# Kernel optimization log

Measured on AMD Instinct MI355X. Metric: run time of the kernel, lower is better.

Reference implementation:

```python
import jax, jax.numpy as jnp
import numpy as np
from jax import lax

B, N, M, K = 8, 4096, 2048, 64   # graphs, points/graph, fps centers/graph (ratio=0.5), max neighbors
R = 0.5                           # radius
F_IN = 64


def setup_inputs() -> dict:
    key = jax.random.key(0)
    ks = jax.random.split(key, 6)
    x = jax.random.normal(ks[0], (B * N, F_IN), jnp.float32)
    pos = jax.random.normal(ks[1], (B * N, 3), jnp.float32)
    batch = jnp.repeat(jnp.arange(B, dtype=jnp.int32), N)  # sorted graph ids
    def lin_w(k, fi, fo):
        return (jax.random.normal(k, (fi, fo), jnp.float32) / np.sqrt(fi)).astype(jnp.float32)
    w1 = lin_w(ks[2], F_IN + 3, 64); b1 = jnp.zeros((64,), jnp.float32)
    w2 = lin_w(ks[3], 64, 64);       b2 = jnp.zeros((64,), jnp.float32)
    w3 = lin_w(ks[4], 64, 128);      b3 = jnp.zeros((128,), jnp.float32)
    return dict(x=x, pos=pos, batch=batch, w1=w1, b1=b1, w2=w2, b2=b2, w3=w3, b3=b3)


def fps(pos_g, m):
    """Farthest point sampling on one graph [n,3] -> m int32 indices (deterministic start at 0)."""
    n = pos_g.shape[0]
    def step(carry, _):
        mind, last = carry
        d = jnp.sum((pos_g - pos_g[last]) ** 2, axis=-1)
        mind = jnp.minimum(mind, d)
        return (mind, jnp.argmax(mind).astype(jnp.int32)), last
    init = (jnp.full((n,), 1e30, jnp.float32), jnp.int32(0))
    _, idx = lax.scan(step, init, None, length=m)
    return idx


def reference(x, pos, batch, w1, b1, w2, b2, w3, b3):
    # batch is sorted with equal-size graphs -> reshape to [B, N, .]
    pos_b = pos.reshape(B, N, 3)
    x_b = x.reshape(B, N, F_IN)

    # fps per graph (PyG.fps with ratio=0.5)
    cidx = jax.vmap(lambda p: fps(p, M))(pos_b)                 # [B, M]
    bi = jnp.arange(B)[:, None]
    pos_c = pos_b[bi, cidx]                                     # [B, M, 3]

    # radius ball query, capped at K neighbors (take K nearest, mask > R)
    d2 = jnp.sum((pos_c[:, :, None, :] - pos_b[:, None, :, :]) ** 2, axis=-1)  # [B, M, N]
    neg_d2k, nbr = lax.top_k(-d2, K)                            # [B, M, K]
    mask = (-neg_d2k) <= R * R                                  # center itself always valid (d=0)

    # PointConv message: nn(concat[x_j, pos_j - pos_i]), then max-aggregate per center
    bii = jnp.arange(B)[:, None, None]
    x_j = x_b[bii, nbr]                                         # [B, M, K, F_IN]
    rel = pos_b[bii, nbr] - pos_c[:, :, None, :]                # [B, M, K, 3]
    h = jnp.concatenate([x_j, rel], axis=-1)                    # [B, M, K, F_IN+3]
    h = jax.nn.relu(h @ w1 + b1)
    h = jax.nn.relu(h @ w2 + b2)
    h = h @ w3 + b3                                             # [B, M, K, 128]
    h = jnp.where(mask[..., None], h, -jnp.inf)
    out = jnp.max(h, axis=2)                                    # [B, M, 128]

    out_x = out.reshape(B * M, 128)
    out_pos = pos_c.reshape(B * M, 3)
    out_batch = jnp.repeat(jnp.arange(B, dtype=jnp.int32), M)
    return out_x, out_pos, out_batch
```

## Files before the change

kernel.cpp:

```cpp
#include <hip/hip_runtime.h>

#define BG 8
#define NP 4096
#define MC 2048
#define KN 64
#define NWK 248
#define CAND 480

__device__ __forceinline__ float dist2(float ax, float ay, float az,
                                       float bx, float by, float bz) {
    float dx = __fsub_rn(ax, bx), dy = __fsub_rn(ay, by), dz = __fsub_rn(az, bz);
    return __fadd_rn(__fadd_rn(__fmul_rn(dx, dx), __fmul_rn(dy, dy)), __fmul_rn(dz, dz));
}

template <int CTRL>
__device__ __forceinline__ float dppmax(float v) {
    int t = __builtin_amdgcn_update_dpp(0, __float_as_int(v), CTRL, 0xf, 0xf, true);
    return fmaxf(v, __int_as_float(t));
}

__global__ __launch_bounds__(256) void k_pre(
    const float* __restrict__ x, const float* __restrict__ w1, const float* __restrict__ b1,
    float* __restrict__ y)
{
    __shared__ float smem[8384];
    const int tid = threadIdx.x;
    const int p0 = blockIdx.x * 64;
    float* xs = smem;
    float* wsm = smem + 4160;
    float* bsm = smem + 8256;
    for (int i = tid; i < 4096; i += 256) {
        xs[(i >> 6) * 65 + (i & 63)] = x[(size_t)p0 * 64 + i];
        wsm[i] = w1[i];
    }
    if (tid < 64) bsm[tid] = b1[tid];
    __syncthreads();
    const int pl = tid >> 2, oq = tid & 3;
    float acc[16];
    #pragma unroll
    for (int u = 0; u < 16; u++) acc[u] = bsm[oq * 16 + u];
    for (int f = 0; f < 64; f++) {
        float xv = xs[pl * 65 + f];
        const float4* wp = (const float4*)&wsm[f * 64 + oq * 16];
        float4 a = wp[0], b4 = wp[1], c4 = wp[2], d4 = wp[3];
        acc[0] = fmaf(xv, a.x, acc[0]);   acc[1] = fmaf(xv, a.y, acc[1]);
        acc[2] = fmaf(xv, a.z, acc[2]);   acc[3] = fmaf(xv, a.w, acc[3]);
        acc[4] = fmaf(xv, b4.x, acc[4]);  acc[5] = fmaf(xv, b4.y, acc[5]);
        acc[6] = fmaf(xv, b4.z, acc[6]);  acc[7] = fmaf(xv, b4.w, acc[7]);
        acc[8] = fmaf(xv, c4.x, acc[8]);  acc[9] = fmaf(xv, c4.y, acc[9]);
        acc[10] = fmaf(xv, c4.z, acc[10]); acc[11] = fmaf(xv, c4.w, acc[11]);
        acc[12] = fmaf(xv, d4.x, acc[12]); acc[13] = fmaf(xv, d4.y, acc[13]);
        acc[14] = fmaf(xv, d4.z, acc[14]); acc[15] = fmaf(xv, d4.w, acc[15]);
    }
    float4* yo = (float4*)&y[((size_t)p0 + pl) * 64 + oq * 16];
    yo[0] = make_float4(acc[0], acc[1], acc[2], acc[3]);
    yo[1] = make_float4(acc[4], acc[5], acc[6], acc[7]);
    yo[2] = make_float4(acc[8], acc[9], acc[10], acc[11]);
    yo[3] = make_float4(acc[12], acc[13], acc[14], acc[15]);
}

__global__ __launch_bounds__(512, 2) void k_fused(
    const float* __restrict__ pos, const float* __restrict__ y,
    const float* __restrict__ w1, const float* __restrict__ w2, const float* __restrict__ b2,
    const float* __restrict__ w3, const float* __restrict__ b3,
    float* __restrict__ out_pos, float* __restrict__ out_batch, float* __restrict__ out_x,
    int* __restrict__ prog)
{
    __shared__ float smem[12320];
    const int tid = threadIdx.x;
    if (blockIdx.x < BG) {
        const int b = blockIdx.x;
        const float* pg = pos + (size_t)b * NP * 3;
        for (int i = tid; i < NP * 3; i += 512) smem[i] = pg[i];
        __syncthreads();
        const int lane = tid & 63, wv = tid >> 6;
        float px[8], py[8], pz[8], mind[8];
        const int base = tid * 8;
        #pragma unroll
        for (int i = 0; i < 8; i++) {
            px[i] = smem[(base + i) * 3];
            py[i] = smem[(base + i) * 3 + 1];
            pz[i] = smem[(base + i) * 3 + 2];
            mind[i] = 1e30f;
        }
        float2* sl = (float2*)(smem + NP * 3);
        float cx = smem[0], cy = smem[1], cz = smem[2];
        if (tid == 0) {
            const size_t c3 = (size_t)b * MC * 3;
            __hip_atomic_store(&out_pos[c3 + 0], cx, __ATOMIC_RELAXED, __HIP_MEMORY_SCOPE_AGENT);
            __hip_atomic_store(&out_pos[c3 + 1], cy, __ATOMIC_RELAXED, __HIP_MEMORY_SCOPE_AGENT);
            __hip_atomic_store(&out_pos[c3 + 2], cz, __ATOMIC_RELAXED, __HIP_MEMORY_SCOPE_AGENT);
        }
        for (int m = 1; m < MC; m++) {
            float bv = -1.0f; int bi = base;
            #pragma unroll
            for (int i = 0; i < 8; i++) {
                float d = dist2(px[i], py[i], pz[i], cx, cy, cz);
                float nm = fminf(mind[i], d);
                mind[i] = nm;
                if (nm > bv) { bv = nm; bi = base + i; }
            }
            float v = bv;
            v = dppmax<0x111>(v);
            v = dppmax<0x112>(v);
            v = dppmax<0x114>(v);
            v = dppmax<0x118>(v);
            v = dppmax<0x142>(v);
            v = dppmax<0x143>(v);
            const float V = __int_as_float(__builtin_amdgcn_readlane(__float_as_int(v), 63));
            unsigned long long mk = __ballot(bv == V);
            float2* sb = sl + (m & 1) * 8;
            if (lane == (int)(__ffsll((long long)mk) - 1))
                sb[wv] = make_float2(V, __int_as_float(bi));
            __syncthreads();
            const float4* sq = (const float4*)sb;
            float4 q0 = sq[0], q1 = sq[1], q2 = sq[2], q3 = sq[3];
            float Vg = q0.x; int ig = __float_as_int(q0.y);
            if (q0.z > Vg) { Vg = q0.z; ig = __float_as_int(q0.w); }
            if (q1.x > Vg) { Vg = q1.x; ig = __float_as_int(q1.y); }
            if (q1.z > Vg) { Vg = q1.z; ig = __float_as_int(q1.w); }
            if (q2.x > Vg) { Vg = q2.x; ig = __float_as_int(q2.y); }
            if (q2.z > Vg) { Vg = q2.z; ig = __float_as_int(q2.w); }
            if (q3.x > Vg) { Vg = q3.x; ig = __float_as_int(q3.y); }
            if (q3.z > Vg) { Vg = q3.z; ig = __float_as_int(q3.w); }
            cx = smem[ig * 3]; cy = smem[ig * 3 + 1]; cz = smem[ig * 3 + 2];
            if (tid == 0) {
                const size_t c3 = (size_t)(b * MC + m) * 3;
                __hip_atomic_store(&out_pos[c3 + 0], cx, __ATOMIC_RELAXED, __HIP_MEMORY_SCOPE_AGENT);
                __hip_atomic_store(&out_pos[c3 + 1], cy, __ATOMIC_RELAXED, __HIP_MEMORY_SCOPE_AGENT);
                __hip_atomic_store(&out_pos[c3 + 2], cz, __ATOMIC_RELAXED, __HIP_MEMORY_SCOPE_AGENT);
                __hip_atomic_store(&prog[b], m, __ATOMIC_RELAXED, __HIP_MEMORY_SCOPE_AGENT);
            }
        }
        __syncthreads();
        if (tid == 0)
            __hip_atomic_store(&prog[b], MC, __ATOMIC_RELEASE, __HIP_MEMORY_SCOPE_AGENT);
        for (int i = tid; i < MC; i += 512) out_batch[b * MC + i] = (float)b;
    } else {
        const int w = blockIdx.x - BG;
        const int g = w & 7;
        const int sub = w >> 3;
        const int lane = tid & 63, ww = tid >> 6;
        const int waveid = sub * 8 + ww;
        float2* cand = (float2*)smem + ww * CAND;
        int* nlist = (int*)(smem + 7680) + ww * 64;
        float* st1 = smem + 8192 + ww * 136;
        float* st2 = st1 + 68;
        float w2c[64], w3a[64], w3b[64];
        #pragma unroll
        for (int f = 0; f < 64; f++) {
            w2c[f] = w2[f * 64 + lane];
            w3a[f] = w3[f * 128 + lane];
            w3b[f] = w3[f * 128 + 64 + lane];
        }
        const float b2v = b2[lane], b3av = b3[lane], b3bv = b3[lane + 64];
        const float wp0 = w1[64 * 64 + lane], wp1 = w1[65 * 64 + lane], wp2 = w1[66 * 64 + lane];
        const float* pg = pos + (size_t)g * NP * 3;
        const float* yg = y + (size_t)g * NP * 64;
        for (int m = waveid; m < MC; m += NWK) {
            while (__hip_atomic_load(&prog[g], __ATOMIC_ACQUIRE, __HIP_MEMORY_SCOPE_AGENT) <= m) {
                __builtin_amdgcn_s_sleep(8);
            }
            const int ci = g * MC + m;
            const size_t c3 = (size_t)ci * 3;
            const float cx = __hip_atomic_load(&out_pos[c3 + 0], __ATOMIC_RELAXED, __HIP_MEMORY_SCOPE_AGENT);
            const float cy = __hip_atomic_load(&out_pos[c3 + 1], __ATOMIC_RELAXED, __HIP_MEMORY_SCOPE_AGENT);
            const float cz = __hip_atomic_load(&out_pos[c3 + 2], __ATOMIC_RELAXED, __HIP_MEMORY_SCOPE_AGENT);
            int cnt = 0;
            for (int c = 0; c < 64; c++) {
                const int p = c * 64 + lane;
                float ppx = pg[p * 3], ppy = pg[p * 3 + 1], ppz = pg[p * 3 + 2];
                float d2 = dist2(ppx, ppy, ppz, cx, cy, cz);
                bool inr = d2 <= 0.25f;
                unsigned long long mk = __ballot(inr);
                int pre = __popcll(mk & ((1ull << lane) - 1ull));
                int wp = cnt + pre;
                if (inr && wp < CAND) cand[wp] = make_float2(d2, __int_as_float(p));
                cnt += __popcll(mk);
            }
            if (cnt > CAND) cnt = CAND;
            int kc;
            if (cnt <= KN) {
                kc = cnt;
                if (lane < cnt) nlist[lane] = __float_as_int(cand[lane].y);
            } else {
                kc = KN;
                for (int basej = 0; basej < cnt; basej += 64) {
                    int jj = basej + lane;
                    float dj = 3.4e38f; int ij = 0x7fffffff;
                    bool act = jj < cnt;
                    if (act) { float2 e = cand[jj]; dj = e.x; ij = __float_as_int(e.y); }
                    int rank = 0;
                    for (int l = 0; l < cnt; l++) {
                        float2 e = cand[l];
                        float dl = e.x; int il = __float_as_int(e.y);
                        if (dl < dj || (dl == dj && il < ij)) rank++;
                    }
                    if (act && rank < KN) nlist[rank] = ij;
                }
            }
            float mA = -3.4e38f, mB = -3.4e38f;
            for (int k = 0; k < kc; k++) {
                const int j = nlist[k];
                const float yv = yg[(size_t)j * 64 + lane];
                const float jx = pg[j * 3], jy = pg[j * 3 + 1], jz = pg[j * 3 + 2];
                float rx = jx - cx, ry = jy - cy, rz = jz - cz;
                float h1 = fmaf(rx, wp0, yv);
                h1 = fmaf(ry, wp1, h1);
                h1 = fmaf(rz, wp2, h1);
                h1 = fmaxf(h1, 0.f);
                st1[lane] = h1;
                float a2a = b2v, a2b = 0.f;
                #pragma unroll
                for (int fc = 0; fc < 16; fc += 2) {
                    float4 hA = *(const float4*)&st1[fc * 4];
                    float4 hB = *(const float4*)&st1[fc * 4 + 4];
                    a2a = fmaf(hA.x, w2c[fc * 4], a2a);
                    a2a = fmaf(hA.y, w2c[fc * 4 + 1], a2a);
                    a2a = fmaf(hA.z, w2c[fc * 4 + 2], a2a);
                    a2a = fmaf(hA.w, w2c[fc * 4 + 3], a2a);
                    a2b = fmaf(hB.x, w2c[fc * 4 + 4], a2b);
                    a2b = fmaf(hB.y, w2c[fc * 4 + 5], a2b);
                    a2b = fmaf(hB.z, w2c[fc * 4 + 6], a2b);
                    a2b = fmaf(hB.w, w2c[fc * 4 + 7], a2b);
                }
                float h2 = fmaxf(a2a + a2b, 0.f);
                st2[lane] = h2;
                float a3 = b3av, a4 = b3bv;
                #pragma unroll
                for (int fc = 0; fc < 16; fc++) {
                    float4 h = *(const float4*)&st2[fc * 4];
                    a3 = fmaf(h.x, w3a[fc * 4], a3);
                    a3 = fmaf(h.y, w3a[fc * 4 + 1], a3);
                    a3 = fmaf(h.z, w3a[fc * 4 + 2], a3);
                    a3 = fmaf(h.w, w3a[fc * 4 + 3], a3);
                    a4 = fmaf(h.x, w3b[fc * 4], a4);
                    a4 = fmaf(h.y, w3b[fc * 4 + 1], a4);
                    a4 = fmaf(h.z, w3b[fc * 4 + 2], a4);
                    a4 = fmaf(h.w, w3b[fc * 4 + 3], a4);
                }
                mA = fmaxf(mA, a3);
                mB = fmaxf(mB, a4);
            }
            out_x[(size_t)ci * 128 + lane] = mA;
            out_x[(size_t)ci * 128 + 64 + lane] = mB;
        }
    }
}

extern "C" void kernel_launch(void* const* d_in, const int* in_sizes, int n_in,
                              void* d_out, int out_size, void* d_ws, size_t ws_size,
                              hipStream_t stream) {
    const float* x   = (const float*)d_in[0];
    const float* pos = (const float*)d_in[1];
    const float* w1  = (const float*)d_in[3];
    const float* b1  = (const float*)d_in[4];
    const float* w2  = (const float*)d_in[5];
    const float* b2  = (const float*)d_in[6];
    const float* w3  = (const float*)d_in[7];
    const float* b3  = (const float*)d_in[8];

    float* out_x     = (float*)d_out;
    float* out_pos   = out_x + (size_t)BG * MC * 128;
    float* out_batch = out_pos + (size_t)BG * MC * 3;

    char* ws  = (char*)d_ws;
    float* y  = (float*)ws;
    int* prog = (int*)(ws + 8388608);

    hipMemsetAsync(prog, 0, 8 * sizeof(int), stream);
    hipLaunchKernelGGL(k_pre, dim3(512), dim3(256), 0, stream, x, w1, b1, y);
    hipLaunchKernelGGL(k_fused, dim3(256), dim3(512), 0, stream,
                       pos, y, w1, w2, b2, w3, b3, out_pos, out_batch, out_x, prog);
}
```

Measured before the change: 1.670 ms.

## Fuse first-layer projection into worker blocks of persistent FPS kernel

Removes the separate k_pre launch. The 248 worker blocks now compute the x@w1 projection for a slice of points while the 8 FPS blocks run, then wait on a per-graph counter until all 31 worker blocks for that graph have finished before they start neighbor processing. Progress counters are padded to separate cache lines, and the spin-wait uses relaxed loads with a sleep length that adapts to how far behind FPS is. Shared memory is doubled and launch bounds drop to 1 block per CU, which may reduce occupancy. The new cross-block dependency relies on all blocks being co-resident.

```diff
diff --git a/kernel.cpp b/kernel.cpp
--- a/kernel.cpp
+++ b/kernel.cpp
@@ -19,54 +19,16 @@
     return fmaxf(v, __int_as_float(t));
 }
 
-__global__ __launch_bounds__(256) void k_pre(
-    const float* __restrict__ x, const float* __restrict__ w1, const float* __restrict__ b1,
-    float* __restrict__ y)
+__global__ __launch_bounds__(512, 1) void k_fused(
+    const float* __restrict__ pos, const float* __restrict__ x,
+    const float* __restrict__ w1, const float* __restrict__ b1,
+    const float* __restrict__ w2, const float* __restrict__ b2,
+    const float* __restrict__ w3, const float* __restrict__ b3,
+    float* __restrict__ y,
+    float* __restrict__ out_pos, float* __restrict__ out_batch, float* __restrict__ out_x,
+    int* __restrict__ prog, int* __restrict__ yready)
 {
-    __shared__ float smem[8384];
-    const int tid = threadIdx.x;
-    const int p0 = blockIdx.x * 64;
-    float* xs = smem;
-    float* wsm = smem + 4160;
-    float* bsm = smem + 8256;
-    for (int i = tid; i < 4096; i += 256) {
-        xs[(i >> 6) * 65 + (i & 63)] = x[(size_t)p0 * 64 + i];
-        wsm[i] = w1[i];
-    }
-    if (tid < 64) bsm[tid] = b1[tid];
-    __syncthreads();
-    const int pl = tid >> 2, oq = tid & 3;
-    float acc[16];
-    #pragma unroll
-    for (int u = 0; u < 16; u++) acc[u] = bsm[oq * 16 + u];
-    for (int f = 0; f < 64; f++) {
-        float xv = xs[pl * 65 + f];
-        const float4* wp = (const float4*)&wsm[f * 64 + oq * 16];
-        float4 a = wp[0], b4 = wp[1], c4 = wp[2], d4 = wp[3];
-        acc[0] = fmaf(xv, a.x, acc[0]);   acc[1] = fmaf(xv, a.y, acc[1]);
-        acc[2] = fmaf(xv, a.z, acc[2]);   acc[3] = fmaf(xv, a.w, acc[3]);
-        acc[4] = fmaf(xv, b4.x, acc[4]);  acc[5] = fmaf(xv, b4.y, acc[5]);
-        acc[6] = fmaf(xv, b4.z, acc[6]);  acc[7] = fmaf(xv, b4.w, acc[7]);
-        acc[8] = fmaf(xv, c4.x, acc[8]);  acc[9] = fmaf(xv, c4.y, acc[9]);
-        acc[10] = fmaf(xv, c4.z, acc[10]); acc[11] = fmaf(xv, c4.w, acc[11]);
-        acc[12] = fmaf(xv, d4.x, acc[12]); acc[13] = fmaf(xv, d4.y, acc[13]);
-        acc[14] = fmaf(xv, d4.z, acc[14]); acc[15] = fmaf(xv, d4.w, acc[15]);
-    }
-    float4* yo = (float4*)&y[((size_t)p0 + pl) * 64 + oq * 16];
-    yo[0] = make_float4(acc[0], acc[1], acc[2], acc[3]);
-    yo[1] = make_float4(acc[4], acc[5], acc[6], acc[7]);
-    yo[2] = make_float4(acc[8], acc[9], acc[10], acc[11]);
-    yo[3] = make_float4(acc[12], acc[13], acc[14], acc[15]);
-}
-
-__global__ __launch_bounds__(512, 2) void k_fused(
-    const float* __restrict__ pos, const float* __restrict__ y,
-    const float* __restrict__ w1, const float* __restrict__ w2, const float* __restrict__ b2,
-    const float* __restrict__ w3, const float* __restrict__ b3,
-    float* __restrict__ out_pos, float* __restrict__ out_batch, float* __restrict__ out_x,
-    int* __restrict__ prog)
-{
-    __shared__ float smem[12320];
+    __shared__ float smem[24576];
     const int tid = threadIdx.x;
     if (blockIdx.x < BG) {
         const int b = blockIdx.x;
@@ -129,12 +91,12 @@
                 __hip_atomic_store(&out_pos[c3 + 0], cx, __ATOMIC_RELAXED, __HIP_MEMORY_SCOPE_AGENT);
                 __hip_atomic_store(&out_pos[c3 + 1], cy, __ATOMIC_RELAXED, __HIP_MEMORY_SCOPE_AGENT);
                 __hip_atomic_store(&out_pos[c3 + 2], cz, __ATOMIC_RELAXED, __HIP_MEMORY_SCOPE_AGENT);
-                __hip_atomic_store(&prog[b], m, __ATOMIC_RELAXED, __HIP_MEMORY_SCOPE_AGENT);
+                __hip_atomic_store(&prog[b * 16], m, __ATOMIC_RELAXED, __HIP_MEMORY_SCOPE_AGENT);
             }
         }
         __syncthreads();
         if (tid == 0)
-            __hip_atomic_store(&prog[b], MC, __ATOMIC_RELEASE, __HIP_MEMORY_SCOPE_AGENT);
+            __hip_atomic_store(&prog[b * 16], MC, __ATOMIC_RELEASE, __HIP_MEMORY_SCOPE_AGENT);
         for (int i = tid; i < MC; i += 512) out_batch[b * MC + i] = (float)b;
     } else {
         const int w = blockIdx.x - BG;
@@ -142,10 +104,27 @@
         const int sub = w >> 3;
         const int lane = tid & 63, ww = tid >> 6;
         const int waveid = sub * 8 + ww;
-        float2* cand = (float2*)smem + ww * CAND;
-        int* nlist = (int*)(smem + 7680) + ww * 64;
-        float* st1 = smem + 8192 + ww * 136;
-        float* st2 = st1 + 68;
+        float* wsm = smem;
+        for (int i = tid; i < 4096; i += 512) wsm[i] = w1[i];
+        const float b1v = b1[lane];
+        __syncthreads();
+        const int p0 = sub * 133;
+        const int p1 = (p0 + 133 < NP) ? p0 + 133 : NP;
+        const float* xg = x + (size_t)g * NP * 64;
+        float* yg_w = y + (size_t)g * NP * 64;
+        for (int p = p0 + ww; p < p1; p += 8) {
+            float xrow = xg[(size_t)p * 64 + lane];
+            float acc = b1v;
+            #pragma unroll
+            for (int f = 0; f < 64; f++) {
+                float xf = __shfl(xrow, f, 64);
+                acc = fmaf(xf, wsm[f * 64 + lane], acc);
+            }
+            yg_w[(size_t)p * 64 + lane] = acc;
+        }
+        __syncthreads();
+        if (tid == 0)
+            __hip_atomic_fetch_add(&yready[g * 16], 1, __ATOMIC_RELEASE, __HIP_MEMORY_SCOPE_AGENT);
         float w2c[64], w3a[64], w3b[64];
         #pragma unroll
         for (int f = 0; f < 64; f++) {
@@ -155,11 +134,23 @@
         }
         const float b2v = b2[lane], b3av = b3[lane], b3bv = b3[lane + 64];
         const float wp0 = w1[64 * 64 + lane], wp1 = w1[65 * 64 + lane], wp2 = w1[66 * 64 + lane];
+        while (__hip_atomic_load(&yready[g * 16], __ATOMIC_RELAXED, __HIP_MEMORY_SCOPE_AGENT) < 31)
+            __builtin_amdgcn_s_sleep(16);
+        {
+            int yr = __hip_atomic_load(&yready[g * 16], __ATOMIC_ACQUIRE, __HIP_MEMORY_SCOPE_AGENT);
+            asm volatile("" :: "v"(yr));
+        }
+        float2* cand = (float2*)(smem + 4096) + ww * CAND;
+        int* nlist = (int*)(smem + 11776) + ww * 64;
+        float* st1 = smem + 12288 + ww * 136;
+        float* st2 = st1 + 68;
         const float* pg = pos + (size_t)g * NP * 3;
         const float* yg = y + (size_t)g * NP * 64;
         for (int m = waveid; m < MC; m += NWK) {
-            while (__hip_atomic_load(&prog[g], __ATOMIC_ACQUIRE, __HIP_MEMORY_SCOPE_AGENT) <= m) {
-                __builtin_amdgcn_s_sleep(8);
+            int cur;
+            while ((cur = __hip_atomic_load(&prog[g * 16], __ATOMIC_RELAXED, __HIP_MEMORY_SCOPE_AGENT)) <= m) {
+                if (m - cur > 16) __builtin_amdgcn_s_sleep(64);
+                else              __builtin_amdgcn_s_sleep(4);
             }
             const int ci = g * MC + m;
             const size_t c3 = (size_t)ci * 3;
@@ -264,12 +255,13 @@
     float* out_pos   = out_x + (size_t)BG * MC * 128;
     float* out_batch = out_pos + (size_t)BG * MC * 3;
 
-    char* ws  = (char*)d_ws;
-    float* y  = (float*)ws;
-    int* prog = (int*)(ws + 8388608);
-
-    hipMemsetAsync(prog, 0, 8 * sizeof(int), stream);
-    hipLaunchKernelGGL(k_pre, dim3(512), dim3(256), 0, stream, x, w1, b1, y);
+    char* ws    = (char*)d_ws;
+    float* y    = (float*)ws;
+    int* prog   = (int*)(ws + 8388608);
+    int* yready = (int*)(ws + 8389120);
+
+    (void)hipMemsetAsync(prog, 0, 1024, stream);
     hipLaunchKernelGGL(k_fused, dim3(256), dim3(512), 0, stream,
-                       pos, y, w1, w2, b2, w3, b3, out_pos, out_batch, out_x, prog);
-}
+                       pos, x, w1, b1, w2, b2, w3, b3,
+                       y, out_pos, out_batch, out_x, prog, yready);
+}
```

New measurement: 1.364 ms. -18.3%, faster.
